# Performance work log

Measured on AMD Instinct MI355X. Metric: run time of the kernel, lower is better.

The kernel has to match this reference:

```python
import jax, jax.numpy as jnp
import numpy as np

N_SRC = 200000
N_DST = 50000
N_EDGES = 800000
N_IN = 256
N_OUT = 128


def setup_inputs() -> dict:
    key = jax.random.key(0)
    ks = jax.random.split(key, 10)
    x = jax.random.normal(ks[0], (N_SRC, N_IN), dtype=jnp.float32)
    edge_rows = jax.random.randint(ks[1], (N_EDGES,), 0, N_DST, dtype=jnp.int32)
    edge_cols = jax.random.randint(ks[2], (N_EDGES,), 0, N_SRC, dtype=jnp.int32)
    edge_vals = jax.random.uniform(ks[3], (N_EDGES,), dtype=jnp.float32)
    sampled_nodes = jax.random.randint(ks[4], (N_DST,), 0, N_SRC, dtype=jnp.int32)
    W_w = jax.random.normal(ks[5], (N_IN, N_OUT), dtype=jnp.float32) * 0.05
    b_w = jax.random.normal(ks[6], (N_OUT,), dtype=jnp.float32) * 0.05
    W_b = jax.random.normal(ks[7], (N_IN, N_OUT), dtype=jnp.float32) * 0.05
    b_b = jax.random.normal(ks[8], (N_OUT,), dtype=jnp.float32) * 0.05
    scale = jnp.ones((2 * N_OUT,), dtype=jnp.float32)
    offset = jnp.zeros((2 * N_OUT,), dtype=jnp.float32)
    return {"x": x, "edge_rows": edge_rows, "edge_cols": edge_cols,
            "edge_vals": edge_vals, "sampled_nodes": sampled_nodes,
            "W_w": W_w, "b_w": b_w, "W_b": W_b, "b_b": b_b,
            "scale": scale, "offset": offset}


def reference(x, edge_rows, edge_cols, edge_vals, sampled_nodes,
              W_w, b_w, W_b, b_b, scale, offset):
    # SpMM: feat[r] = sum_e vals[e] * x[cols[e]] for rows[e]==r  -> [N_DST, N_IN]
    msgs = edge_vals[:, None] * x[edge_cols]
    feat = jax.ops.segment_sum(msgs, edge_rows, num_segments=N_DST)
    # dual linear + concat -> [N_DST, 2*N_OUT]
    self_part = x[sampled_nodes] @ W_b + b_b
    neigh_part = feat @ W_w + b_w
    out = jax.nn.elu(jnp.concatenate([self_part, neigh_part], axis=1))
    # row-wise normalize (biased variance), then affine
    mean = out.mean(axis=1, keepdims=True)
    var = out.var(axis=1, keepdims=True) + 1e-9
    return (out - mean) * scale * jax.lax.rsqrt(var) + offset
```

## Files before the change

kernel.cpp:

```cpp
#include <hip/hip_runtime.h>
#include <math.h>

#define N_SRC   200000
#define N_DST   50000
#define N_EDGES 800000
#define N_IN    256
#define N_OUT   128
#define CAP     64

#define WS_CNT   0
#define WS_WTW   204800
#define WS_WTB   270336
#define WS_SELF  335872
#define WS_Y     13135872
#define WS_CSR   64335872

typedef short  bf16x8 __attribute__((ext_vector_type(8)));
typedef unsigned short u16x8 __attribute__((ext_vector_type(8)));
typedef float  f32x4  __attribute__((ext_vector_type(4)));

__device__ inline unsigned short f2bf(float f) {
    unsigned u = __builtin_bit_cast(unsigned, f);
    u += 0x7fffu + ((u >> 16) & 1u);
    return (unsigned short)(u >> 16);
}
__device__ inline float bf2f(unsigned short h) {
    return __builtin_bit_cast(float, (unsigned)h << 16);
}

__global__ __launch_bounds__(256) void k_init(const float* __restrict__ Ww,
                                              const float* __restrict__ Wb,
                                              unsigned short* __restrict__ Wtw,
                                              unsigned short* __restrict__ Wtb,
                                              int* __restrict__ cnt) {
    int tot = blockIdx.x * 256 + threadIdx.x;
    int sel = tot >> 15;
    int idx = tot & 32767;
    int n = idx >> 8, k = idx & 255;
    const float* src = sel ? Wb : Ww;
    unsigned short* dst = sel ? Wtb : Wtw;
    dst[n * 256 + k] = f2bf(src[k * 128 + n]);
    if (tot < N_DST) cnt[tot] = 0;
}

#define GSCAT 3125
#define GBIG  3125
#define GSELF 782
#define LDT 88
#define EPS 132
__global__ __launch_bounds__(256) void k_mega(
        const float* __restrict__ x,
        const int* __restrict__ erows, const int* __restrict__ ecols,
        const float* __restrict__ evals, const int* __restrict__ sn,
        const unsigned short* __restrict__ Wtw, const unsigned short* __restrict__ Wtb,
        int* __restrict__ cnt, int2* __restrict__ csr_pad,
        unsigned short* __restrict__ ybuf, unsigned short* __restrict__ selfp) {
    __shared__ __align__(16) unsigned short smA[64 * LDT];
    __shared__ __align__(16) unsigned short smB[128 * LDT];
    const int tid = threadIdx.x;

    if (blockIdx.x < GSCAT) {
        int i = blockIdx.x * 256 + tid;
        int r = erows[i];
        int rank = atomicAdd(&cnt[r], 1);
        if (rank < CAP) {
            int2 cv;
            cv.x = ecols[i];
            cv.y = __builtin_bit_cast(int, evals[i]);
            csr_pad[r * CAP + rank] = cv;
        }
        return;
    }

    const int gb = blockIdx.x - GSCAT;
    const bool isBig = gb < GBIG;
    const int* rowidx = isBig ? nullptr : sn;
    const unsigned short* Bt = isBig ? Wtw : Wtb;
    unsigned short* Y = isBig ? ybuf : selfp;
    const int M = isBig ? N_SRC : N_DST;
    const int bid = isBig ? gb : gb - GBIG;

    const int lane = tid & 63, wid = tid >> 6;
    const int l15 = lane & 15, quad = lane >> 4;
    const int row0 = bid * 64;

    const int ar = tid >> 2, aseg = (tid & 3) * 16;
    int srow = row0 + ar;
    if (srow >= M) srow = M - 1;
    if (rowidx) srow = rowidx[srow];
    const float* aptr = x + (long)srow * 256 + aseg;
    const int bn = tid >> 1, bhalf = (tid & 1) * 32;
    const unsigned short* bptr = Bt + (long)bn * 256 + bhalf;

    f32x4 acc[8];
    #pragma unroll
    for (int t = 0; t < 8; t++) acc[t] = (f32x4){0.f, 0.f, 0.f, 0.f};

    for (int kt = 0; kt < 4; kt++) {
        const int k0 = kt * 64;
        {
            const float4* s4 = (const float4*)(aptr + k0);
            float4 v0 = s4[0], v1 = s4[1], v2 = s4[2], v3 = s4[3];
            u16x8 w0, w1;
            w0[0]=f2bf(v0.x); w0[1]=f2bf(v0.y); w0[2]=f2bf(v0.z); w0[3]=f2bf(v0.w);
            w0[4]=f2bf(v1.x); w0[5]=f2bf(v1.y); w0[6]=f2bf(v1.z); w0[7]=f2bf(v1.w);
            w1[0]=f2bf(v2.x); w1[1]=f2bf(v2.y); w1[2]=f2bf(v2.z); w1[3]=f2bf(v2.w);
            w1[4]=f2bf(v3.x); w1[5]=f2bf(v3.y); w1[6]=f2bf(v3.z); w1[7]=f2bf(v3.w);
            *(u16x8*)&smA[ar * LDT + aseg]     = w0;
            *(u16x8*)&smA[ar * LDT + aseg + 8] = w1;
        }
        {
            const u16x8* s8 = (const u16x8*)(bptr + k0);
            u16x8 b0 = s8[0], b1 = s8[1], b2 = s8[2], b3 = s8[3];
            *(u16x8*)&smB[bn * LDT + bhalf]      = b0;
            *(u16x8*)&smB[bn * LDT + bhalf + 8]  = b1;
            *(u16x8*)&smB[bn * LDT + bhalf + 16] = b2;
            *(u16x8*)&smB[bn * LDT + bhalf + 24] = b3;
        }
        __syncthreads();
        #pragma unroll
        for (int ks = 0; ks < 64; ks += 32) {
            bf16x8 af = *(const bf16x8*)&smA[(wid * 16 + l15) * LDT + ks + quad * 8];
            #pragma unroll
            for (int t = 0; t < 8; t++) {
                bf16x8 bf = *(const bf16x8*)&smB[(t * 16 + l15) * LDT + ks + quad * 8];
                acc[t] = __builtin_amdgcn_mfma_f32_16x16x32_bf16(af, bf, acc[t], 0, 0, 0);
            }
        }
        __syncthreads();
    }

    #pragma unroll
    for (int t = 0; t < 8; t++)
        #pragma unroll
        for (int rg = 0; rg < 4; rg++)
            smB[(wid * 16 + quad * 4 + rg) * EPS + t * 16 + l15] = f2bf(acc[t][rg]);
    __syncthreads();
    const int orow = tid >> 2, oc0 = (tid & 3) * 32;
    if (row0 + orow < M) {
        unsigned short* dst = Y + (long)(row0 + orow) * 128 + oc0;
        #pragma unroll
        for (int i = 0; i < 4; i++)
            *(u16x8*)(dst + i * 8) = *(const u16x8*)&smB[orow * EPS + oc0 + i * 8];
    }
}

__global__ __launch_bounds__(256) void k_sage(const unsigned short* __restrict__ y,
                                              const unsigned short* __restrict__ selfp,
                                              const int* __restrict__ cnt,
                                              const int2* __restrict__ csr_pad,
                                              const float* __restrict__ bw,
                                              const float* __restrict__ bb,
                                              const float* __restrict__ scale,
                                              const float* __restrict__ offs,
                                              float* __restrict__ out) {
    const int tid = threadIdx.x, lane = tid & 63, wid = tid >> 6;
    const int row = blockIdx.x * 4 + wid;
    const int m = min(cnt[row], CAP);

    int2 cv = (lane < m) ? csr_pad[(long)row * CAP + lane] : make_int2(0, 0);

    unsigned spk = *(const unsigned*)(selfp + (long)row * 128 + lane * 2);
    float s0 = bf2f((unsigned short)(spk & 0xffff)) + bb[lane * 2];
    float s1 = bf2f((unsigned short)(spk >> 16))    + bb[lane * 2 + 1];
    s0 = s0 > 0.f ? s0 : expm1f(s0);
    s1 = s1 > 0.f ? s1 : expm1f(s1);

    float a0 = 0.f, a1 = 0.f;
    for (int e = 0; e < m; e++) {
        int   c = __shfl(cv.x, e, 64);
        float v = __builtin_bit_cast(float, __shfl(cv.y, e, 64));
        unsigned pk = *(const unsigned*)(y + (long)c * 128 + lane * 2);
        a0 = fmaf(v, __builtin_bit_cast(float, pk << 16), a0);
        a1 = fmaf(v, __builtin_bit_cast(float, pk & 0xffff0000u), a1);
    }
    a0 += bw[lane * 2];
    a1 += bw[lane * 2 + 1];
    a0 = a0 > 0.f ? a0 : expm1f(a0);
    a1 = a1 > 0.f ? a1 : expm1f(a1);

    float s  = s0 + s1 + a0 + a1;
    float s2 = s0 * s0 + s1 * s1 + a0 * a0 + a1 * a1;
    #pragma unroll
    for (int o = 32; o > 0; o >>= 1) {
        s  += __shfl_xor(s,  o, 64);
        s2 += __shfl_xor(s2, o, 64);
    }
    float mean = s * (1.f / 256.f);
    float var  = s2 * (1.f / 256.f) - mean * mean;
    float rstd = rsqrtf(var + 1e-9f);

    float* orow = out + (long)row * 256;
    float2 w0, w1;
    w0.x = (s0 - mean) * rstd * scale[lane * 2]           + offs[lane * 2];
    w0.y = (s1 - mean) * rstd * scale[lane * 2 + 1]       + offs[lane * 2 + 1];
    w1.x = (a0 - mean) * rstd * scale[128 + lane * 2]     + offs[128 + lane * 2];
    w1.y = (a1 - mean) * rstd * scale[128 + lane * 2 + 1] + offs[128 + lane * 2 + 1];
    *(float2*)(orow + lane * 2)       = w0;
    *(float2*)(orow + 128 + lane * 2) = w1;
}

extern "C" void kernel_launch(void* const* d_in, const int* in_sizes, int n_in,
                              void* d_out, int out_size, void* d_ws, size_t ws_size,
                              hipStream_t stream) {
    const float* x     = (const float*)d_in[0];
    const int*   erows = (const int*)  d_in[1];
    const int*   ecols = (const int*)  d_in[2];
    const float* evals = (const float*)d_in[3];
    const int*   sn    = (const int*)  d_in[4];
    const float* Ww    = (const float*)d_in[5];
    const float* bw    = (const float*)d_in[6];
    const float* Wb    = (const float*)d_in[7];
    const float* bb    = (const float*)d_in[8];
    const float* scale = (const float*)d_in[9];
    const float* offs  = (const float*)d_in[10];
    float* out = (float*)d_out;

    char* ws = (char*)d_ws;
    int*   cnt     = (int*)  (ws + WS_CNT);
    unsigned short* Wtw   = (unsigned short*)(ws + WS_WTW);
    unsigned short* Wtb   = (unsigned short*)(ws + WS_WTB);
    unsigned short* selfp = (unsigned short*)(ws + WS_SELF);
    unsigned short* ybuf  = (unsigned short*)(ws + WS_Y);
    int2*  csr_pad = (int2*) (ws + WS_CSR);

    k_init <<<256, 256, 0, stream>>>(Ww, Wb, Wtw, Wtb, cnt);
    k_mega <<<GSCAT + GBIG + GSELF, 256, 0, stream>>>(x, erows, ecols, evals, sn,
                                                      Wtw, Wtb, cnt, csr_pad, ybuf, selfp);
    k_sage <<<N_DST / 4, 256, 0, stream>>>(ybuf, selfp, cnt, csr_pad,
                                           bw, bb, scale, offs, out);
}
```

Before: 448.3 us.

## Shrink GEMM K-tile to raise occupancy and batch edge gathers in SpMM

```diff
diff --git a/kernel.cpp b/kernel.cpp
--- a/kernel.cpp
+++ b/kernel.cpp
@@ -46,17 +46,19 @@
 #define GSCAT 3125
 #define GBIG  3125
 #define GSELF 782
-#define LDT 88
+#define LDA 40
 #define EPS 132
-__global__ __launch_bounds__(256) void k_mega(
+
+__global__ __launch_bounds__(256, 8) void k_mega(
         const float* __restrict__ x,
         const int* __restrict__ erows, const int* __restrict__ ecols,
         const float* __restrict__ evals, const int* __restrict__ sn,
         const unsigned short* __restrict__ Wtw, const unsigned short* __restrict__ Wtb,
         int* __restrict__ cnt, int2* __restrict__ csr_pad,
         unsigned short* __restrict__ ybuf, unsigned short* __restrict__ selfp) {
-    __shared__ __align__(16) unsigned short smA[64 * LDT];
-    __shared__ __align__(16) unsigned short smB[128 * LDT];
+    __shared__ __align__(16) unsigned short sm[8448];
+    unsigned short* smA = sm;
+    unsigned short* smB = sm + 2560;
     const int tid = threadIdx.x;
 
     if (blockIdx.x < GSCAT) {
@@ -84,48 +86,44 @@
     const int l15 = lane & 15, quad = lane >> 4;
     const int row0 = bid * 64;
 
-    const int ar = tid >> 2, aseg = (tid & 3) * 16;
+    const int ar = tid >> 2, aseg = (tid & 3) * 8;
     int srow = row0 + ar;
     if (srow >= M) srow = M - 1;
     if (rowidx) srow = rowidx[srow];
     const float* aptr = x + (long)srow * 256 + aseg;
-    const int bn = tid >> 1, bhalf = (tid & 1) * 32;
-    const unsigned short* bptr = Bt + (long)bn * 256 + bhalf;
+    const int bn = tid >> 1, bh = (tid & 1) * 16;
+    const unsigned short* bptr = Bt + (long)bn * 256 + bh;
+
+    unsigned short* smAw = &smA[ar * LDA + aseg];
+    unsigned short* smBw = &smB[bn * LDA + bh];
+    const unsigned short* smAr = &smA[(wid * 16 + l15) * LDA + quad * 8];
 
     f32x4 acc[8];
     #pragma unroll
     for (int t = 0; t < 8; t++) acc[t] = (f32x4){0.f, 0.f, 0.f, 0.f};
 
-    for (int kt = 0; kt < 4; kt++) {
-        const int k0 = kt * 64;
+    for (int kt = 0; kt < 8; kt++) {
+        const int k0 = kt * 32;
         {
             const float4* s4 = (const float4*)(aptr + k0);
-            float4 v0 = s4[0], v1 = s4[1], v2 = s4[2], v3 = s4[3];
-            u16x8 w0, w1;
-            w0[0]=f2bf(v0.x); w0[1]=f2bf(v0.y); w0[2]=f2bf(v0.z); w0[3]=f2bf(v0.w);
-            w0[4]=f2bf(v1.x); w0[5]=f2bf(v1.y); w0[6]=f2bf(v1.z); w0[7]=f2bf(v1.w);
-            w1[0]=f2bf(v2.x); w1[1]=f2bf(v2.y); w1[2]=f2bf(v2.z); w1[3]=f2bf(v2.w);
-            w1[4]=f2bf(v3.x); w1[5]=f2bf(v3.y); w1[6]=f2bf(v3.z); w1[7]=f2bf(v3.w);
-            *(u16x8*)&smA[ar * LDT + aseg]     = w0;
-            *(u16x8*)&smA[ar * LDT + aseg + 8] = w1;
+            float4 v0 = s4[0], v1 = s4[1];
+            u16x8 w;
+            w[0]=f2bf(v0.x); w[1]=f2bf(v0.y); w[2]=f2bf(v0.z); w[3]=f2bf(v0.w);
+            w[4]=f2bf(v1.x); w[5]=f2bf(v1.y); w[6]=f2bf(v1.z); w[7]=f2bf(v1.w);
+            *(u16x8*)smAw = w;
         }
         {
             const u16x8* s8 = (const u16x8*)(bptr + k0);
-            u16x8 b0 = s8[0], b1 = s8[1], b2 = s8[2], b3 = s8[3];
-            *(u16x8*)&smB[bn * LDT + bhalf]      = b0;
-            *(u16x8*)&smB[bn * LDT + bhalf + 8]  = b1;
-            *(u16x8*)&smB[bn * LDT + bhalf + 16] = b2;
-            *(u16x8*)&smB[bn * LDT + bhalf + 24] = b3;
+            u16x8 b0 = s8[0], b1 = s8[1];
+            *(u16x8*)smBw       = b0;
+            *(u16x8*)(smBw + 8) = b1;
         }
         __syncthreads();
+        bf16x8 af = *(const bf16x8*)smAr;
         #pragma unroll
-        for (int ks = 0; ks < 64; ks += 32) {
-            bf16x8 af = *(const bf16x8*)&smA[(wid * 16 + l15) * LDT + ks + quad * 8];
-            #pragma unroll
-            for (int t = 0; t < 8; t++) {
-                bf16x8 bf = *(const bf16x8*)&smB[(t * 16 + l15) * LDT + ks + quad * 8];
-                acc[t] = __builtin_amdgcn_mfma_f32_16x16x32_bf16(af, bf, acc[t], 0, 0, 0);
-            }
+        for (int t = 0; t < 8; t++) {
+            bf16x8 bfv = *(const bf16x8*)&smB[(t * 16 + l15) * LDA + quad * 8];
+            acc[t] = __builtin_amdgcn_mfma_f32_16x16x32_bf16(af, bfv, acc[t], 0, 0, 0);
         }
         __syncthreads();
     }
@@ -134,16 +132,24 @@
     for (int t = 0; t < 8; t++)
         #pragma unroll
         for (int rg = 0; rg < 4; rg++)
-            smB[(wid * 16 + quad * 4 + rg) * EPS + t * 16 + l15] = f2bf(acc[t][rg]);
+            sm[(wid * 16 + quad * 4 + rg) * EPS + t * 16 + l15] = f2bf(acc[t][rg]);
     __syncthreads();
     const int orow = tid >> 2, oc0 = (tid & 3) * 32;
     if (row0 + orow < M) {
         unsigned short* dst = Y + (long)(row0 + orow) * 128 + oc0;
         #pragma unroll
         for (int i = 0; i < 4; i++)
-            *(u16x8*)(dst + i * 8) = *(const u16x8*)&smB[orow * EPS + oc0 + i * 8];
-    }
-}
+            *(u16x8*)(dst + i * 8) = *(const u16x8*)&sm[orow * EPS + oc0 + i * 8];
+    }
+}
+
+#define GATHER(j) \
+    int   c##j = __shfl(cv.x, e0 + j, 64); \
+    float v##j = __builtin_bit_cast(float, __shfl(cv.y, e0 + j, 64)); \
+    unsigned p##j = *(const unsigned*)(y + (long)c##j * 128 + (lane << 1));
+#define ACCUM(j) \
+    a0 = fmaf(v##j, __builtin_bit_cast(float, p##j << 16), a0); \
+    a1 = fmaf(v##j, __builtin_bit_cast(float, p##j & 0xffff0000u), a1);
 
 __global__ __launch_bounds__(256) void k_sage(const unsigned short* __restrict__ y,
                                               const unsigned short* __restrict__ selfp,
@@ -167,12 +173,12 @@
     s1 = s1 > 0.f ? s1 : expm1f(s1);
 
     float a0 = 0.f, a1 = 0.f;
-    for (int e = 0; e < m; e++) {
-        int   c = __shfl(cv.x, e, 64);
-        float v = __builtin_bit_cast(float, __shfl(cv.y, e, 64));
-        unsigned pk = *(const unsigned*)(y + (long)c * 128 + lane * 2);
-        a0 = fmaf(v, __builtin_bit_cast(float, pk << 16), a0);
-        a1 = fmaf(v, __builtin_bit_cast(float, pk & 0xffff0000u), a1);
+    const int mm = (m + 7) & ~7;
+    for (int e0 = 0; e0 < mm; e0 += 8) {
+        GATHER(0) GATHER(1) GATHER(2) GATHER(3)
+        GATHER(4) GATHER(5) GATHER(6) GATHER(7)
+        ACCUM(0) ACCUM(1) ACCUM(2) ACCUM(3)
+        ACCUM(4) ACCUM(5) ACCUM(6) ACCUM(7)
     }
     a0 += bw[lane * 2];
     a1 += bw[lane * 2 + 1];
```

After: 421.1 us. 6.1% less time.
